# Kernel optimization log

Hardware: AMD Instinct MI355X
Metric: run time of the kernel (lower is better)

Reference implementation:

```python
import jax, jax.numpy as jnp
import numpy as np

B, T, C, H, N = 2, 1024, 1024, 16, 64
D_DECAY, D_AAA, D_MV, D_GATE = 64, 64, 32, 128
LN_EPS = 64e-5  # GroupNorm eps used by RWKV7 (1e-5 * head_size_divisor**2)


def setup_inputs():
    key = jax.random.key(0)
    ks = jax.random.split(key, 32)
    rn = lambda k, shape, s=1.0: jax.random.normal(k, shape, jnp.float32) * s
    p = {}
    p['x'] = rn(ks[0], (B, T, C))
    p['v_first'] = rn(ks[1], (B, T, C))
    for i, nm in enumerate(['x_r', 'x_w', 'x_k', 'x_v', 'x_a', 'x_g']):
        p[nm] = jax.random.uniform(ks[2 + i], (1, 1, C), jnp.float32)
    p['w1'] = rn(ks[8], (C, D_DECAY), 0.02); p['w2'] = rn(ks[9], (D_DECAY, C), 0.02); p['w0'] = rn(ks[10], (C,), 0.5)
    p['a1'] = rn(ks[11], (C, D_AAA), 0.02); p['a2'] = rn(ks[12], (D_AAA, C), 0.02); p['a0'] = rn(ks[13], (C,), 0.1)
    p['v1'] = rn(ks[14], (C, D_MV), 0.02); p['v2'] = rn(ks[15], (D_MV, C), 0.02); p['v0'] = rn(ks[16], (C,), 0.1)
    p['g1'] = rn(ks[17], (C, D_GATE), 0.02); p['g2'] = rn(ks[18], (D_GATE, C), 0.02)
    p['k_k'] = jax.random.uniform(ks[19], (1, 1, C), jnp.float32)
    p['k_a'] = jax.random.uniform(ks[20], (1, 1, C), jnp.float32)
    p['r_k'] = rn(ks[21], (H, N), 0.1)
    s = C ** -0.5
    p['W_r'] = rn(ks[22], (C, C), s); p['W_k'] = rn(ks[23], (C, C), s)
    p['W_v'] = rn(ks[24], (C, C), s); p['W_o'] = rn(ks[25], (C, C), s)
    p['ln_w'] = jnp.ones((C,), jnp.float32); p['ln_b'] = jnp.zeros((C,), jnp.float32)
    return p


def _rwkv7_op(r, w, k, v, a, b):
    # r,w,k,v,a,b: (B,T,C). Per-head matrix-state recurrence:
    #   S_t = S_{t-1} * diag(decay_t) + (S_{t-1} @ a_t) b_t^T + v_t k_t^T ; out_t = S_t @ r_t
    f = lambda z: z.reshape(B, T, H, N).astype(jnp.float32).transpose(1, 0, 2, 3)  # (T,B,H,N)
    r_, k_, v_, a_, b_ = f(r), f(k), f(v), f(a), f(b)
    d_ = jnp.exp(-jnp.exp(f(w)))  # decay in (0,1)

    def step(S, inp):
        rt, dt, kt, vt, at, bt = inp  # each (B,H,N)
        sa = jnp.einsum('bhij,bhj->bhi', S, at)
        S = S * dt[:, :, None, :] + sa[..., None] * bt[:, :, None, :] + vt[..., None] * kt[:, :, None, :]
        return S, jnp.einsum('bhij,bhj->bhi', S, rt)

    S0 = jnp.zeros((B, H, N, N), jnp.float32)
    _, out = jax.lax.scan(step, S0, (r_, d_, k_, v_, a_, b_))
    return out.transpose(1, 0, 2, 3).reshape(B, T, C)


def _forward(x, v_first, x_r, x_w, x_k, x_v, x_a, x_g, w1, w2, w0, a1, a2, a0,
             v1, v2, v0, g1, g2, k_k, k_a, r_k, W_r, W_k, W_v, W_o, ln_w, ln_b):
    xx = jnp.pad(x, ((0, 0), (1, 0), (0, 0)))[:, :T] - x  # token shift
    xr = x + xx * x_r; xw = x + xx * x_w; xk = x + xx * x_k
    xv = x + xx * x_v; xa = x + xx * x_a; xg = x + xx * x_g
    r = xr @ W_r
    w = -jax.nn.softplus(-(jnp.tanh(xw @ w1) @ w2 + w0)) - 0.5
    k = xk @ W_k
    v = xv @ W_v
    v = v + (v_first - v) * jax.nn.sigmoid(xv @ v1 @ v2 + v0)  # layer_id > 0 branch
    a = jax.nn.sigmoid(xa @ a1 @ a2 + a0)
    g = jax.nn.sigmoid(xg @ g1) @ g2
    kk = (k * k_k).reshape(B, T, H, N)
    kk = (kk / jnp.maximum(jnp.linalg.norm(kk, axis=-1, keepdims=True), 1e-12)).reshape(B, T, C)
    k = k * (1.0 + (a - 1.0) * k_a)
    y = _rwkv7_op(r, w, k, v, -kk, kk * a)
    # GroupNorm(H groups over C) applied per token
    yh = y.reshape(B, T, H, N)
    mu = yh.mean(-1, keepdims=True)
    var = yh.var(-1, keepdims=True)
    y = ((yh - mu) / jnp.sqrt(var + LN_EPS)).reshape(B, T, C) * ln_w + ln_b
    rh = r.reshape(B, T, H, N); kh = k.reshape(B, T, H, N); vh = v.reshape(B, T, H, N)
    y = y + ((rh * kh * r_k).sum(-1, keepdims=True) * vh).reshape(B, T, C)
    return (y * g) @ W_o


def reference(x, v_first, x_r, x_w, x_k, x_v, x_a, x_g, w1, w2, w0, a1, a2, a0,
              v1, v2, v0, g1, g2, k_k, k_a, r_k, W_r, W_k, W_v, W_o, ln_w, ln_b):
    out = _forward(x, v_first, x_r, x_w, x_k, x_v, x_a, x_g, w1, w2, w0, a1, a2, a0,
                   v1, v2, v0, g1, g2, k_k, k_a, r_k, W_r, W_k, W_v, W_o, ln_w, ln_b)
    return (out, v_first)
```

## Files before the change

kernel.cpp:

```cpp
#include <hip/hip_runtime.h>
#include <hip/hip_bf16.h>
#include <cstdint>
#include <cstddef>

typedef __hip_bfloat16 bf16;
typedef __bf16 bf16x8 __attribute__((ext_vector_type(8)));
typedef float f32x4 __attribute__((ext_vector_type(4)));

#define BB 2
#define TT 1024
#define CC 1024
#define HH 16
#define PKS 448
#define PKB 1792
#define CH 8
#define NCH 4
#define STEPB 2048
#define CHB (CH * STEPB)
#define NC (TT / CH)

__device__ __forceinline__ bf16 f2b(float v){ return __float2bfloat16(v); }

__device__ __forceinline__ float hex_add(float x) {
    x += __int_as_float(__builtin_amdgcn_mov_dpp(__float_as_int(x), 0xB1, 0xF, 0xF, true));
    x += __int_as_float(__builtin_amdgcn_mov_dpp(__float_as_int(x), 0x4E, 0xF, 0xF, true));
    x += __int_as_float(__builtin_amdgcn_mov_dpp(__float_as_int(x), 0x141, 0xF, 0xF, true));
    x += __int_as_float(__builtin_amdgcn_mov_dpp(__float_as_int(x), 0x140, 0xF, 0xF, true));
    return x;
}

typedef __attribute__((address_space(3))) void as3_void;
typedef __attribute__((address_space(1))) const void as1_void;
__device__ __forceinline__ void gload_lds16(const void* g, void* l) {
    __builtin_amdgcn_global_load_lds((as1_void*)g, (as3_void*)l, 16, 0, 0);
}

struct TrDesc { const float* in; bf16* out; int R, S; };
struct PrepArgs {
    TrDesc d[12];
    const float* x; const float* vfirst;
    const float *mr, *mw, *mk, *mv, *ma, *mg;
    bf16 *xr, *xw, *xk, *xv, *xa, *xg;
    float* vout;
};

__global__ __launch_bounds__(256) void prep_kernel(PrepArgs args)
{
    if (blockIdx.z < 12) {
        TrDesc t = args.d[blockIdx.z];
        __shared__ float tile[32][33];
        int s0 = blockIdx.x * 32, r0 = blockIdx.y * 32;
        if (s0 >= t.S || r0 >= t.R) return;
        int tx = threadIdx.x & 31, ty = threadIdx.x >> 5;
#pragma unroll
        for (int i = 0; i < 4; i++) {
            int r = r0 + ty + i * 8, s = s0 + tx;
            if (r < t.R && s < t.S) tile[ty + i * 8][tx] = t.in[(size_t)r * t.S + s];
        }
        __syncthreads();
#pragma unroll
        for (int i = 0; i < 4; i++) {
            int s = s0 + ty + i * 8, r = r0 + tx;
            if (s < t.S && r < t.R) t.out[(size_t)s * t.R + r] = f2b(tile[tx][ty + i * 8]);
        }
        return;
    }
    int bid = blockIdx.y * 32 + blockIdx.x;
#pragma unroll
    for (int rr = 0; rr < 2; rr++) {
        int row = bid * 2 + rr;
        int t = row & (TT - 1);
        size_t base = (size_t)row * CC;
        for (int c = threadIdx.x; c < CC; c += 256) {
            float xc = args.x[base + c];
            float xp = (t > 0) ? args.x[base - CC + c] : 0.f;
            float d = xp - xc;
            args.xr[base + c] = f2b(xc + d * args.mr[c]);
            args.xw[base + c] = f2b(xc + d * args.mw[c]);
            args.xk[base + c] = f2b(xc + d * args.mk[c]);
            args.xv[base + c] = f2b(xc + d * args.mv[c]);
            args.xa[base + c] = f2b(xc + d * args.ma[c]);
            args.xg[base + c] = f2b(xc + d * args.mg[c]);
            args.vout[base + c] = args.vfirst[base + c];
        }
    }
}

template <class EmitF>
__device__ __forceinline__ void gemm_tile(const bf16* __restrict__ A, const bf16* __restrict__ BT,
                                          int K, int m0, int n0, EmitF emit)
{
    __shared__ __align__(16) bf16 Atile[2][128 * 32];
    __shared__ __align__(16) bf16 Btile[2][128 * 32];
    int tid = threadIdx.x;
    int w = tid >> 6, lane = tid & 63;
    int wr = w >> 1, wc = w & 1;
    int quad = lane >> 4, l16 = lane & 15;

    f32x4 zero = {0.f, 0.f, 0.f, 0.f};
    f32x4 acc[4][4];
#pragma unroll
    for (int i = 0; i < 4; i++)
#pragma unroll
        for (int j = 0; j < 4; j++) acc[i][j] = zero;

    int rr = lane >> 2;
    int cs = lane & 3;
    int ra0 = w * 32 + rr;
    int ra1 = ra0 + 16;
    int cg0 = cs ^ ((ra0 >> 1) & 3);
    int cg1 = cs ^ ((ra1 >> 1) & 3);

    const bf16* Ar0 = A  + (size_t)(m0 + ra0) * K + cg0 * 8;
    const bf16* Ar1 = A  + (size_t)(m0 + ra1) * K + cg1 * 8;
    const bf16* Br0 = BT + (size_t)(n0 + ra0) * K + cg0 * 8;
    const bf16* Br1 = BT + (size_t)(n0 + ra1) * K + cg1 * 8;

    auto stage = [&](int k0, int buf) {
        bf16* atb = Atile[buf] + w * 1024;
        bf16* btb = Btile[buf] + w * 1024;
        gload_lds16(Ar0 + k0, atb);
        gload_lds16(Ar1 + k0, atb + 512);
        gload_lds16(Br0 + k0, btb);
        gload_lds16(Br1 + k0, btb + 512);
    };

    stage(0, 0);
    __syncthreads();

    int cur = 0;
    for (int k0 = 0; k0 < K; k0 += 32) {
        if (k0 + 32 < K) stage(k0 + 32, cur ^ 1);

        bf16x8 af[4], bfr[4];
#pragma unroll
        for (int mi = 0; mi < 4; mi++) {
            int m = wr * 64 + mi * 16 + l16;
            int c2 = quad ^ ((m >> 1) & 3);
            af[mi] = *reinterpret_cast<const bf16x8*>(&Atile[cur][m * 32 + c2 * 8]);
        }
#pragma unroll
        for (int ni = 0; ni < 4; ni++) {
            int n = wc * 64 + ni * 16 + l16;
            int c2 = quad ^ ((n >> 1) & 3);
            bfr[ni] = *reinterpret_cast<const bf16x8*>(&Btile[cur][n * 32 + c2 * 8]);
        }
#pragma unroll
        for (int mi = 0; mi < 4; mi++)
#pragma unroll
            for (int ni = 0; ni < 4; ni++)
                acc[mi][ni] = __builtin_amdgcn_mfma_f32_16x16x32_bf16(af[mi], bfr[ni], acc[mi][ni], 0, 0, 0);

        __syncthreads();
        cur ^= 1;
    }

#pragma unroll
    for (int mi = 0; mi < 4; mi++)
#pragma unroll
        for (int ni = 0; ni < 4; ni++)
#pragma unroll
            for (int rg = 0; rg < 4; rg++) {
                int m = m0 + wr * 64 + mi * 16 + quad * 4 + rg;
                int n = n0 + wc * 64 + ni * 16 + l16;
                emit(m, n, acc[mi][ni][rg]);
            }
}

struct L1Desc { const bf16* A; const bf16* BT; bf16* outB; int N; int mode; };
struct ProjArgs { const bf16* A[3]; const bf16* BT[3]; float* out[3]; L1Desc d[4]; };

__global__ __launch_bounds__(256) void proj_kernel(ProjArgs args)
{
    int z = blockIdx.z;
    if (z < 3) {
        float* out = args.out[z];
        gemm_tile(args.A[z], args.BT[z], 1024, blockIdx.x * 128, blockIdx.y * 128,
                  [&](int m, int n, float v) { out[(size_t)m * 1024 + n] = v; });
        return;
    }
    if (blockIdx.y) return;
    L1Desc dz = args.d[z - 3];
    gemm_tile(dz.A, dz.BT, 1024, blockIdx.x * 128, 0,
              [&](int m, int n, float v) {
                  if (n < dz.N) {
                      float r = (dz.mode == 2) ? tanhf(v)
                              : (dz.mode == 3) ? 1.f / (1.f + expf(-v)) : v;
                      dz.outB[(size_t)m * dz.N + n] = f2b(r);
                  }
              });
}

struct L2Desc { const bf16* A; const bf16* BT; const float* bias; float* outF; int K; int mode; };
struct L2Args { L2Desc d[4]; const float* vraw; const float* vfirst; };
__global__ __launch_bounds__(256) void lora2_kernel(L2Args args)
{
    L2Desc dz = args.d[blockIdx.z];
    gemm_tile(dz.A, dz.BT, dz.K, blockIdx.x * 128, blockIdx.y * 128,
              [&](int m, int n, float v) {
                  size_t idx = (size_t)m * 1024 + n;
                  if (dz.mode == 4) {
                      float xx = v + dz.bias[n];
                      float ww = -log1pf(expf(-xx)) - 0.5f;
                      dz.outF[idx] = expf(-expf(ww));
                  } else if (dz.mode == 5) {
                      float xx = v + dz.bias[n];
                      dz.outF[idx] = 1.f / (1.f + expf(-xx));
                  } else if (dz.mode == 6) {
                      float gate = 1.f / (1.f + expf(-(v + dz.bias[n])));
                      float vr = args.vraw[idx];
                      dz.outF[idx] = vr + (args.vfirst[idx] - vr) * gate;
                  } else {
                      dz.outF[idx] = v;
                  }
              });
}

__global__ __launch_bounds__(256) void final_kernel(const bf16* __restrict__ A, const bf16* __restrict__ BT,
                                                    float* __restrict__ out)
{
    gemm_tile(A, BT, 1024, blockIdx.x * 128, blockIdx.y * 128,
              [&](int m, int n, float v) { out[(size_t)m * 1024 + n] = v; });
}

__global__ __launch_bounds__(256) void pack_kernel(
    float* __restrict__ k, const float* __restrict__ a, const float* __restrict__ r,
    const float* __restrict__ v, const float* __restrict__ dw,
    const float* __restrict__ kkw, const float* __restrict__ kaw,
    float* __restrict__ PK)
{
    int tid = threadIdx.x;
    int wave = tid >> 6, lane = tid & 63;
    int idx = blockIdx.x * 4 + wave;
    size_t off = (size_t)idx * 64 + lane;
    int c = (idx & 15) * 64 + lane;
    float kraw = k[off];
    float av = a[off];
    float kkv = kraw * kkw[c];
    float s = kkv * kkv;
#pragma unroll
    for (int m = 32; m; m >>= 1) s += __shfl_xor(s, m);
    float kkn = kkv / fmaxf(sqrtf(s), 1e-12f);
    float ks = kraw * (1.f + (av - 1.f) * kaw[c]);
    k[off] = ks;
    float bb = kkn * av;
    float rv = r[off];
    float dv = dw[off];
    float bt = bb * rv, ct = ks * rv;
#pragma unroll
    for (int m = 32; m; m >>= 1) { bt += __shfl_xor(bt, m); ct += __shfl_xor(ct, m); }
    int b = idx >> 14;
    int h = idx & 15;
    int t = (idx >> 4) & (TT - 1);
    size_t sidx = (size_t)(b * HH + h) * TT + t;
    float* pw = PK + sidx * PKS;
    pw[lane] = ks; pw[64 + lane] = kkn; pw[128 + lane] = bb; pw[192 + lane] = v[off];
    pw[256 + lane] = rv; pw[320 + lane] = dv;
    if (lane == 0) { pw[384] = bt; pw[385] = ct; }
}

struct SetR { f32x4 q, d, r, k, b; float vi; float2 bc; };

__device__ __forceinline__ void ds_load_set(SetR& s, const char* slot, int c16, int row)
{
    s.q  = *(const f32x4*)(slot + 256  + c16);
    s.d  = *(const f32x4*)(slot + 1280 + c16);
    s.r  = *(const f32x4*)(slot + 1024 + c16);
    s.k  = *(const f32x4*)(slot + 0    + c16);
    s.b  = *(const f32x4*)(slot + 512  + c16);
    s.vi = *(const float*)(slot + 768 + row * 4);
    s.bc = *(const float2*)(slot + 1536);
}

__device__ __forceinline__ float step4(const SetR& sd, f32x4& S)
{
    f32x4 Sd   = S * sd.d;
    f32x4 sacv = S * sd.q;
    f32x4 oacv = Sd * sd.r;
    float sar = (sacv[0] + sacv[1]) + (sacv[2] + sacv[3]);
    float od  = (oacv[0] + oacv[1]) + (oacv[2] + oacv[3]);
    sar = hex_add(sar);
    od  = hex_add(od);
    float sa = -sar;
    float o = fmaf(sd.vi, sd.bc.y, fmaf(sa, sd.bc.x, od));
    S = Sd + sa * sd.b + sd.vi * sd.k;
    return o;
}

__global__ __launch_bounds__(256, 1) void scan_kernel(
    const float* __restrict__ PK, float* __restrict__ ybuf)
{
    __shared__ __align__(16) char ring[NCH * CHB];
    const int tid = threadIdx.x;
    const int wid = tid >> 6, lane = tid & 63;
    const int xcd = blockIdx.x & 7, kk = blockIdx.x >> 3;
    const int bh = xcd * 4 + (kk >> 4);
    const int wq = kk & 15;
    const int b = bh >> 4, h = bh & 15;
    const int row = wq * 4 + (lane >> 4);
    const int c = lane & 15;
    const int c16 = c * 16;

    const char* base = (const char*)(PK + (size_t)bh * TT * PKS);
    const char* g1 = base + lane * 16;
    const char* g2 = g1 + 1024;

    auto stage_chunk = [&](int ci) {
        const char* p1 = g1 + (size_t)ci * CH * PKB;
        const char* p2 = g2 + (size_t)ci * CH * PKB;
        char* s = ring + (ci & (NCH - 1)) * CHB;
        for (int j = wid - 1; j < CH; j += 3) {
            gload_lds16(p1 + (size_t)j * PKB, s + j * STEPB);
            gload_lds16(p2 + (size_t)j * PKB, s + j * STEPB + 1024);
        }
    };

    if (wid > 0) {
        stage_chunk(0);
        stage_chunk(1);
        stage_chunk(2);
        asm volatile("s_waitcnt vmcnt(0)" ::: "memory");
    }
    __builtin_amdgcn_sched_barrier(0);
    __builtin_amdgcn_s_barrier();
    __builtin_amdgcn_sched_barrier(0);

    f32x4 S = {0.f, 0.f, 0.f, 0.f};
    SetR X, Y;
    if (wid == 0) ds_load_set(X, ring, c16, row);
    float* py = ybuf + (size_t)b * TT * CC + h * 64 + row;

    for (int i = 0; i < NC; i++) {
        if (wid == 0) {
            const char* sl  = ring + (i & (NCH - 1)) * CHB;
            const char* sln = ring + ((i + 1) & (NCH - 1)) * CHB;
            float o;
            ds_load_set(Y, sl + 1 * STEPB, c16, row); o = step4(X, S); if (c == 0) *py = o; py += CC;
            ds_load_set(X, sl + 2 * STEPB, c16, row); o = step4(Y, S); if (c == 0) *py = o; py += CC;
            ds_load_set(Y, sl + 3 * STEPB, c16, row); o = step4(X, S); if (c == 0) *py = o; py += CC;
            ds_load_set(X, sl + 4 * STEPB, c16, row); o = step4(Y, S); if (c == 0) *py = o; py += CC;
            ds_load_set(Y, sl + 5 * STEPB, c16, row); o = step4(X, S); if (c == 0) *py = o; py += CC;
            ds_load_set(X, sl + 6 * STEPB, c16, row); o = step4(Y, S); if (c == 0) *py = o; py += CC;
            ds_load_set(Y, sl + 7 * STEPB, c16, row); o = step4(X, S); if (c == 0) *py = o; py += CC;
            ds_load_set(X, sln,            c16, row); o = step4(Y, S); if (c == 0) *py = o; py += CC;
        } else {
            if (i + 3 < NC) {
                stage_chunk(i + 3);
                if (wid == 3) asm volatile("s_waitcnt vmcnt(4)" ::: "memory");
                else          asm volatile("s_waitcnt vmcnt(6)" ::: "memory");
            } else {
                asm volatile("s_waitcnt vmcnt(0)" ::: "memory");
            }
        }
        __builtin_amdgcn_sched_barrier(0);
        __builtin_amdgcn_s_barrier();
        __builtin_amdgcn_sched_barrier(0);
    }
}

__global__ __launch_bounds__(256) void gn_kernel(
    const float* __restrict__ y, const float* __restrict__ r, const float* __restrict__ k,
    const float* __restrict__ v, const float* __restrict__ g,
    const float* __restrict__ lnw, const float* __restrict__ lnb,
    const float* __restrict__ rk, bf16* __restrict__ z)
{
    int tid = threadIdx.x;
    int idx = blockIdx.x * 4 + (tid >> 6);
    int lane = tid & 63;
    size_t off = (size_t)idx * 64 + lane;
    int c = (idx & 15) * 64 + lane;
    float yv = y[off];
    float rv = r[off], kv = k[off], vv = v[off];
    float s1 = yv, s2 = yv * yv, s3 = rv * kv * rk[c];
#pragma unroll
    for (int m = 32; m; m >>= 1) {
        s1 += __shfl_xor(s1, m);
        s2 += __shfl_xor(s2, m);
        s3 += __shfl_xor(s3, m);
    }
    float mu = s1 * (1.f / 64.f);
    float var = fmaxf(s2 * (1.f / 64.f) - mu * mu, 0.f);
    float yn = (yv - mu) * rsqrtf(var + 64e-5f) * lnw[c] + lnb[c];
    float out = (yn + s3 * vv) * g[off];
    z[off] = f2b(out);
}

extern "C" void kernel_launch(void* const* d_in, const int* in_sizes, int n_in,
                              void* d_out, int out_size, void* d_ws, size_t ws_size,
                              hipStream_t stream)
{
    const float* x       = (const float*)d_in[0];
    const float* v_first = (const float*)d_in[1];
    const float* x_r = (const float*)d_in[2];
    const float* x_w = (const float*)d_in[3];
    const float* x_k = (const float*)d_in[4];
    const float* x_v = (const float*)d_in[5];
    const float* x_a = (const float*)d_in[6];
    const float* x_g = (const float*)d_in[7];
    const float* w1 = (const float*)d_in[8];
    const float* w2 = (const float*)d_in[9];
    const float* w0 = (const float*)d_in[10];
    const float* a1 = (const float*)d_in[11];
    const float* a2 = (const float*)d_in[12];
    const float* a0 = (const float*)d_in[13];
    const float* v1 = (const float*)d_in[14];
    const float* v2 = (const float*)d_in[15];
    const float* v0 = (const float*)d_in[16];
    const float* g1 = (const float*)d_in[17];
    const float* g2 = (const float*)d_in[18];
    const float* k_k = (const float*)d_in[19];
    const float* k_a = (const float*)d_in[20];
    const float* r_k = (const float*)d_in[21];
    const float* W_r = (const float*)d_in[22];
    const float* W_k = (const float*)d_in[23];
    const float* W_v = (const float*)d_in[24];
    const float* W_o = (const float*)d_in[25];
    const float* ln_w = (const float*)d_in[26];
    const float* ln_b = (const float*)d_in[27];

    const size_t BTC = (size_t)BB * TT * CC;
    const int M = BB * TT;

    char* ws = (char*)d_ws;
    size_t off = 0;
    auto alloc = [&](size_t bytes) -> char* {
        char* p = ws + off;
        off += (bytes + 255) & ~(size_t)255;
        return p;
    };

    bf16* xr = (bf16*)alloc(BTC * 2);
    bf16* xw = (bf16*)alloc(BTC * 2);
    bf16* xk = (bf16*)alloc(BTC * 2);
    bf16* xv = (bf16*)alloc(BTC * 2);
    bf16* xa = (bf16*)alloc(BTC * 2);
    bf16* xg = (bf16*)alloc(BTC * 2);
    bf16* WrT = (bf16*)alloc(1024 * 1024 * 2);
    bf16* WkT = (bf16*)alloc(1024 * 1024 * 2);
    bf16* WvT = (bf16*)alloc(1024 * 1024 * 2);
    bf16* w1T = (bf16*)alloc(128 * 1024 * 2);
    bf16* a1T = (bf16*)alloc(128 * 1024 * 2);
    bf16* v1T = (bf16*)alloc(128 * 1024 * 2);
    bf16* g1T = (bf16*)alloc(128 * 1024 * 2);
    bf16* w2T = (bf16*)alloc(1024 * 64 * 2);
    bf16* a2T = (bf16*)alloc(1024 * 64 * 2);
    bf16* v2T = (bf16*)alloc(1024 * 32 * 2);
    bf16* g2T = (bf16*)alloc(1024 * 128 * 2);
    bf16* h_w = (bf16*)alloc((size_t)M * 64 * 2);
    bf16* h_a = (bf16*)alloc((size_t)M * 64 * 2);
    bf16* h_v = (bf16*)alloc((size_t)M * 32 * 2);
    bf16* h_g = (bf16*)alloc((size_t)M * 128 * 2);

    float* PK = (float*)ws;
    size_t pk_end = (size_t)BB * HH * TT * PKS * 4;
    if (off < pk_end) off = pk_end;
    off = (off + 255) & ~(size_t)255;

    bf16* WoT = (bf16*)alloc(1024 * 1024 * 2);
    float* rbuf = (float*)alloc(BTC * 4);
    float* kbuf = (float*)alloc(BTC * 4);
    float* vraw = (float*)alloc(BTC * 4);
    float* vbuf = (float*)alloc(BTC * 4);
    float* dbuf = (float*)alloc(BTC * 4);
    float* abuf = (float*)alloc(BTC * 4);
    float* gbuf = (float*)alloc(BTC * 4);

    float* ybuf = vraw;
    bf16*  zbuf = (bf16*)dbuf;

    (void)in_sizes; (void)n_in; (void)out_size; (void)ws_size;

    PrepArgs pa;
    pa.d[0]  = {W_r, WrT, 1024, 1024};
    pa.d[1]  = {W_k, WkT, 1024, 1024};
    pa.d[2]  = {W_v, WvT, 1024, 1024};
    pa.d[3]  = {W_o, WoT, 1024, 1024};
    pa.d[4]  = {w1, w1T, 1024, 64};
    pa.d[5]  = {a1, a1T, 1024, 64};
    pa.d[6]  = {v1, v1T, 1024, 32};
    pa.d[7]  = {g1, g1T, 1024, 128};
    pa.d[8]  = {w2, w2T, 64, 1024};
    pa.d[9]  = {a2, a2T, 64, 1024};
    pa.d[10] = {v2, v2T, 32, 1024};
    pa.d[11] = {g2, g2T, 128, 1024};
    pa.x = x; pa.vfirst = v_first;
    pa.mr = x_r; pa.mw = x_w; pa.mk = x_k; pa.mv = x_v; pa.ma = x_a; pa.mg = x_g;
    pa.xr = xr; pa.xw = xw; pa.xk = xk; pa.xv = xv; pa.xa = xa; pa.xg = xg;
    pa.vout = (float*)d_out + BTC;
    prep_kernel<<<dim3(32, 32, 13), 256, 0, stream>>>(pa);

    ProjArgs pj;
    pj.A[0] = xr; pj.A[1] = xk; pj.A[2] = xv;
    pj.BT[0] = WrT; pj.BT[1] = WkT; pj.BT[2] = WvT;
    pj.out[0] = rbuf; pj.out[1] = kbuf; pj.out[2] = vraw;
    pj.d[0] = {xw, w1T, h_w, 64, 2};
    pj.d[1] = {xa, a1T, h_a, 64, 0};
    pj.d[2] = {xv, v1T, h_v, 32, 0};
    pj.d[3] = {xg, g1T, h_g, 128, 3};
    proj_kernel<<<dim3(16, 8, 7), 256, 0, stream>>>(pj);

    L2Args l2;
    l2.d[0] = {h_w, w2T, w0, dbuf, 64, 4};
    l2.d[1] = {h_a, a2T, a0, abuf, 64, 5};
    l2.d[2] = {h_v, v2T, v0, vbuf, 32, 6};
    l2.d[3] = {h_g, g2T, nullptr, gbuf, 128, 0};
    l2.vraw = vraw; l2.vfirst = v_first;
    lora2_kernel<<<dim3(16, 8, 4), 256, 0, stream>>>(l2);

    pack_kernel<<<BB * TT * HH / 4, 256, 0, stream>>>(kbuf, abuf, rbuf, vbuf, dbuf, k_k, k_a, PK);

    scan_kernel<<<BB * HH * 16, 256, 0, stream>>>(PK, ybuf);

    gn_kernel<<<BB * TT * HH / 4, 256, 0, stream>>>(ybuf, rbuf, kbuf, vbuf, gbuf, ln_w, ln_b, r_k, zbuf);

    final_kernel<<<dim3(16, 8), 256, 0, stream>>>(zbuf, WoT, (float*)d_out);
}
```

Baseline: 412.8 us.

## Split scan state across two compute waves with two loader waves

The recurrence scan now uses two compute wavefronts instead of one. Each lane holds 2 state columns instead of 4, and 32 lanes cover a row, with an extra shfl_xor step to finish each reduction. The global-to-LDS staging moves from three producer waves to two, and the vmcnt waits are adjusted to match. This shortens the per-step serial arithmetic chain in the latency-bound scan, at the cost of an extra cross-lane shuffle per reduction and fewer loader waves.

```diff
diff --git a/kernel.cpp b/kernel.cpp
--- a/kernel.cpp
+++ b/kernel.cpp
@@ -6,6 +6,7 @@
 typedef __hip_bfloat16 bf16;
 typedef __bf16 bf16x8 __attribute__((ext_vector_type(8)));
 typedef float f32x4 __attribute__((ext_vector_type(4)));
+typedef float f32x2 __attribute__((ext_vector_type(2)));
 
 #define BB 2
 #define TT 1024
@@ -259,28 +260,28 @@
     if (lane == 0) { pw[384] = bt; pw[385] = ct; }
 }
 
-struct SetR { f32x4 q, d, r, k, b; float vi; float2 bc; };
-
-__device__ __forceinline__ void ds_load_set(SetR& s, const char* slot, int c16, int row)
-{
-    s.q  = *(const f32x4*)(slot + 256  + c16);
-    s.d  = *(const f32x4*)(slot + 1280 + c16);
-    s.r  = *(const f32x4*)(slot + 1024 + c16);
-    s.k  = *(const f32x4*)(slot + 0    + c16);
-    s.b  = *(const f32x4*)(slot + 512  + c16);
+struct SetR2 { f32x2 q, d, r, k, b; float vi; float2 bc; };
+
+__device__ __forceinline__ void ds_load_set2(SetR2& s, const char* slot, int c8, int row)
+{
+    s.q  = *(const f32x2*)(slot + 256  + c8);
+    s.d  = *(const f32x2*)(slot + 1280 + c8);
+    s.r  = *(const f32x2*)(slot + 1024 + c8);
+    s.k  = *(const f32x2*)(slot + 0    + c8);
+    s.b  = *(const f32x2*)(slot + 512  + c8);
     s.vi = *(const float*)(slot + 768 + row * 4);
     s.bc = *(const float2*)(slot + 1536);
 }
 
-__device__ __forceinline__ float step4(const SetR& sd, f32x4& S)
-{
-    f32x4 Sd   = S * sd.d;
-    f32x4 sacv = S * sd.q;
-    f32x4 oacv = Sd * sd.r;
-    float sar = (sacv[0] + sacv[1]) + (sacv[2] + sacv[3]);
-    float od  = (oacv[0] + oacv[1]) + (oacv[2] + oacv[3]);
-    sar = hex_add(sar);
-    od  = hex_add(od);
+__device__ __forceinline__ float step2(const SetR2& sd, f32x2& S)
+{
+    f32x2 Sd   = S * sd.d;
+    f32x2 sacv = S * sd.q;
+    f32x2 oacv = Sd * sd.r;
+    float sar = sacv[0] + sacv[1];
+    float od  = oacv[0] + oacv[1];
+    sar = hex_add(sar); sar += __shfl_xor(sar, 16);
+    od  = hex_add(od);  od  += __shfl_xor(od, 16);
     float sa = -sar;
     float o = fmaf(sd.vi, sd.bc.y, fmaf(sa, sd.bc.x, od));
     S = Sd + sa * sd.b + sd.vi * sd.k;
@@ -297,9 +298,9 @@
     const int bh = xcd * 4 + (kk >> 4);
     const int wq = kk & 15;
     const int b = bh >> 4, h = bh & 15;
-    const int row = wq * 4 + (lane >> 4);
-    const int c = lane & 15;
-    const int c16 = c * 16;
+    const int row = wq * 4 + wid * 2 + (lane >> 5);
+    const int c = lane & 31;
+    const int c8 = c * 8;
 
     const char* base = (const char*)(PK + (size_t)bh * TT * PKS);
     const char* g1 = base + lane * 16;
@@ -309,13 +310,13 @@
         const char* p1 = g1 + (size_t)ci * CH * PKB;
         const char* p2 = g2 + (size_t)ci * CH * PKB;
         char* s = ring + (ci & (NCH - 1)) * CHB;
-        for (int j = wid - 1; j < CH; j += 3) {
+        for (int j = wid - 2; j < CH; j += 2) {
             gload_lds16(p1 + (size_t)j * PKB, s + j * STEPB);
             gload_lds16(p2 + (size_t)j * PKB, s + j * STEPB + 1024);
         }
     };
 
-    if (wid > 0) {
+    if (wid >= 2) {
         stage_chunk(0);
         stage_chunk(1);
         stage_chunk(2);
@@ -325,29 +326,28 @@
     __builtin_amdgcn_s_barrier();
     __builtin_amdgcn_sched_barrier(0);
 
-    f32x4 S = {0.f, 0.f, 0.f, 0.f};
-    SetR X, Y;
-    if (wid == 0) ds_load_set(X, ring, c16, row);
+    f32x2 S = {0.f, 0.f};
+    SetR2 X, Y;
+    if (wid < 2) ds_load_set2(X, ring, c8, row);
     float* py = ybuf + (size_t)b * TT * CC + h * 64 + row;
 
     for (int i = 0; i < NC; i++) {
-        if (wid == 0) {
+        if (wid < 2) {
             const char* sl  = ring + (i & (NCH - 1)) * CHB;
             const char* sln = ring + ((i + 1) & (NCH - 1)) * CHB;
             float o;
-            ds_load_set(Y, sl + 1 * STEPB, c16, row); o = step4(X, S); if (c == 0) *py = o; py += CC;
-            ds_load_set(X, sl + 2 * STEPB, c16, row); o = step4(Y, S); if (c == 0) *py = o; py += CC;
-            ds_load_set(Y, sl + 3 * STEPB, c16, row); o = step4(X, S); if (c == 0) *py = o; py += CC;
-            ds_load_set(X, sl + 4 * STEPB, c16, row); o = step4(Y, S); if (c == 0) *py = o; py += CC;
-            ds_load_set(Y, sl + 5 * STEPB, c16, row); o = step4(X, S); if (c == 0) *py = o; py += CC;
-            ds_load_set(X, sl + 6 * STEPB, c16, row); o = step4(Y, S); if (c == 0) *py = o; py += CC;
-            ds_load_set(Y, sl + 7 * STEPB, c16, row); o = step4(X, S); if (c == 0) *py = o; py += CC;
-            ds_load_set(X, sln,            c16, row); o = step4(Y, S); if (c == 0) *py = o; py += CC;
+            ds_load_set2(Y, sl + 1 * STEPB, c8, row); o = step2(X, S); if (c == 0) *py = o; py += CC;
+            ds_load_set2(X, sl + 2 * STEPB, c8, row); o = step2(Y, S); if (c == 0) *py = o; py += CC;
+            ds_load_set2(Y, sl + 3 * STEPB, c8, row); o = step2(X, S); if (c == 0) *py = o; py += CC;
+            ds_load_set2(X, sl + 4 * STEPB, c8, row); o = step2(Y, S); if (c == 0) *py = o; py += CC;
+            ds_load_set2(Y, sl + 5 * STEPB, c8, row); o = step2(X, S); if (c == 0) *py = o; py += CC;
+            ds_load_set2(X, sl + 6 * STEPB, c8, row); o = step2(Y, S); if (c == 0) *py = o; py += CC;
+            ds_load_set2(Y, sl + 7 * STEPB, c8, row); o = step2(X, S); if (c == 0) *py = o; py += CC;
+            ds_load_set2(X, sln,            c8, row); o = step2(Y, S); if (c == 0) *py = o; py += CC;
         } else {
             if (i + 3 < NC) {
                 stage_chunk(i + 3);
-                if (wid == 3) asm volatile("s_waitcnt vmcnt(4)" ::: "memory");
-                else          asm volatile("s_waitcnt vmcnt(6)" ::: "memory");
+                asm volatile("s_waitcnt vmcnt(8)" ::: "memory");
             } else {
                 asm volatile("s_waitcnt vmcnt(0)" ::: "memory");
             }
```

Result: slower. 435.6 us (+5.5%).

## Fuse two recurrence steps per scan iteration via precomputed pair coefficients

Applied to the files above, without the earlier changes.

The pack kernel now precomputes algebraically combined coefficients for pairs of consecutive timesteps (combined decay, cross terms between the two a/b vectors, merged k and r terms). The scan kernel then advances the state two tokens per iteration, with three reductions plus one for the second output instead of two reductions per token. This halves the number of serial state updates on the latency-bound single-wave scan path. In exchange, each staged record is larger (768 floats per pair), the pack kernel does more shuffles and arithmetic, and rounding differs from the step-by-step update.

```diff
diff --git a/kernel.cpp b/kernel.cpp
--- a/kernel.cpp
+++ b/kernel.cpp
@@ -11,13 +11,12 @@
 #define TT 1024
 #define CC 1024
 #define HH 16
-#define PKS 448
-#define PKB 1792
-#define CH 8
+#define NP 512
+#define PRB 3072
+#define CH 4
 #define NCH 4
-#define STEPB 2048
-#define CHB (CH * STEPB)
-#define NC (TT / CH)
+#define CHB (CH * PRB)
+#define NC (NP / CH)
 
 __device__ __forceinline__ bf16 f2b(float v){ return __float2bfloat16(v); }
 
@@ -232,59 +231,83 @@
     int tid = threadIdx.x;
     int wave = tid >> 6, lane = tid & 63;
     int idx = blockIdx.x * 4 + wave;
-    size_t off = (size_t)idx * 64 + lane;
-    int c = (idx & 15) * 64 + lane;
-    float kraw = k[off];
-    float av = a[off];
-    float kkv = kraw * kkw[c];
-    float s = kkv * kkv;
-#pragma unroll
-    for (int m = 32; m; m >>= 1) s += __shfl_xor(s, m);
-    float kkn = kkv / fmaxf(sqrtf(s), 1e-12f);
-    float ks = kraw * (1.f + (av - 1.f) * kaw[c]);
-    k[off] = ks;
-    float bb = kkn * av;
-    float rv = r[off];
-    float dv = dw[off];
-    float bt = bb * rv, ct = ks * rv;
-#pragma unroll
-    for (int m = 32; m; m >>= 1) { bt += __shfl_xor(bt, m); ct += __shfl_xor(ct, m); }
-    int b = idx >> 14;
-    int h = idx & 15;
-    int t = (idx >> 4) & (TT - 1);
-    size_t sidx = (size_t)(b * HH + h) * TT + t;
-    float* pw = PK + sidx * PKS;
-    pw[lane] = ks; pw[64 + lane] = kkn; pw[128 + lane] = bb; pw[192 + lane] = v[off];
-    pw[256 + lane] = rv; pw[320 + lane] = dv;
-    if (lane == 0) { pw[384] = bt; pw[385] = ct; }
-}
-
-struct SetR { f32x4 q, d, r, k, b; float vi; float2 bc; };
-
-__device__ __forceinline__ void ds_load_set(SetR& s, const char* slot, int c16, int row)
-{
-    s.q  = *(const f32x4*)(slot + 256  + c16);
-    s.d  = *(const f32x4*)(slot + 1280 + c16);
-    s.r  = *(const f32x4*)(slot + 1024 + c16);
-    s.k  = *(const f32x4*)(slot + 0    + c16);
-    s.b  = *(const f32x4*)(slot + 512  + c16);
-    s.vi = *(const float*)(slot + 768 + row * 4);
-    s.bc = *(const float2*)(slot + 1536);
-}
-
-__device__ __forceinline__ float step4(const SetR& sd, f32x4& S)
-{
-    f32x4 Sd   = S * sd.d;
-    f32x4 sacv = S * sd.q;
-    f32x4 oacv = Sd * sd.r;
-    float sar = (sacv[0] + sacv[1]) + (sacv[2] + sacv[3]);
-    float od  = (oacv[0] + oacv[1]) + (oacv[2] + oacv[3]);
-    sar = hex_add(sar);
-    od  = hex_add(od);
-    float sa = -sar;
-    float o = fmaf(sd.vi, sd.bc.y, fmaf(sa, sd.bc.x, od));
-    S = Sd + sa * sd.b + sd.vi * sd.k;
-    return o;
+    int b  = idx >> 13;
+    int tp = (idx >> 4) & (NP - 1);
+    int h  = idx & 15;
+    size_t off0 = ((size_t)(b * TT + 2 * tp) * HH + h) * 64 + lane;
+    size_t off1 = off0 + 1024;
+    float kkw_l = kkw[h * 64 + lane];
+    float kaw_l = kaw[h * 64 + lane];
+
+    float k0 = k[off0], a0 = a[off0], r0 = r[off0], v0 = v[off0], d0 = dw[off0];
+    float k1 = k[off1], a1 = a[off1], r1 = r[off1], v1 = v[off1], d1 = dw[off1];
+
+    float kk0 = k0 * kkw_l, kk1 = k1 * kkw_l;
+    float ks0 = k0 * fmaf(a0 - 1.f, kaw_l, 1.f);
+    float ks1 = k1 * fmaf(a1 - 1.f, kaw_l, 1.f);
+    k[off0] = ks0; k[off1] = ks1;
+
+    float s0 = kk0 * kk0, s1 = kk1 * kk1;
+#pragma unroll
+    for (int m = 32; m; m >>= 1) { s0 += __shfl_xor(s0, m); s1 += __shfl_xor(s1, m); }
+    float kn0 = kk0 / fmaxf(sqrtf(s0), 1e-12f);
+    float kn1 = kk1 / fmaxf(sqrtf(s1), 1e-12f);
+    float A0 = -kn0, A1 = -kn1;
+    float B0 = kn0 * a0, B1 = kn1 * a1;
+
+    float cBA = B0 * A1, cKA = ks0 * A1, beta = B0 * r0, gamma = ks0 * r0;
+#pragma unroll
+    for (int m = 32; m; m >>= 1) {
+        cBA += __shfl_xor(cBA, m); cKA += __shfl_xor(cKA, m);
+        beta += __shfl_xor(beta, m); gamma += __shfl_xor(gamma, m);
+    }
+
+    float At = fmaf(cBA, A0, d0 * A1);
+    float Bt = d1 * B0;
+    float kt = fmaf(cKA, B1, d1 * ks0);
+    float rt = d0 * r0;
+    float d2 = d0 * d1;
+
+    size_t sidx = ((size_t)(b * HH + h) * NP + tp);
+    float* pw = PK + sidx * 768;
+    pw[lane] = kt;        pw[64 + lane]  = ks1;
+    pw[128 + lane] = A0;  pw[192 + lane] = At;
+    pw[256 + lane] = Bt;  pw[320 + lane] = B1;
+    pw[384 + lane] = rt;  pw[448 + lane] = r1;
+    pw[512 + lane] = d2;  pw[576 + lane] = v0;  pw[640 + lane] = v1;
+    if (lane == 0) { pw[704] = beta; pw[705] = gamma; }
+}
+
+struct SetP { f32x4 kt, k1, A, At, Bt, B1, rt, r1, d2; float v0, v1; float2 bg; };
+
+__device__ __forceinline__ void ds_load_pair(SetP& s, const char* slot, int c16, int row)
+{
+    s.A  = *(const f32x4*)(slot + 512  + c16);
+    s.At = *(const f32x4*)(slot + 768  + c16);
+    s.rt = *(const f32x4*)(slot + 1536 + c16);
+    s.d2 = *(const f32x4*)(slot + 2048 + c16);
+    s.Bt = *(const f32x4*)(slot + 1024 + c16);
+    s.B1 = *(const f32x4*)(slot + 1280 + c16);
+    s.kt = *(const f32x4*)(slot + 0    + c16);
+    s.k1 = *(const f32x4*)(slot + 256  + c16);
+    s.r1 = *(const f32x4*)(slot + 1792 + c16);
+    s.v0 = *(const float*)(slot + 2304 + row * 4);
+    s.v1 = *(const float*)(slot + 2560 + row * 4);
+    s.bg = *(const float2*)(slot + 2816);
+}
+
+__device__ __forceinline__ void step_pair(const SetP& sd, f32x4& S, float& o1, float& o2)
+{
+    f32x4 pv = S * sd.A;
+    f32x4 qv = S * sd.At;
+    f32x4 rv = S * sd.rt;
+    float p  = hex_add((pv[0] + pv[1]) + (pv[2] + pv[3]));
+    float q  = hex_add((qv[0] + qv[1]) + (qv[2] + qv[3]));
+    float ro = hex_add((rv[0] + rv[1]) + (rv[2] + rv[3]));
+    o1 = fmaf(sd.v0, sd.bg.y, fmaf(p, sd.bg.x, ro));
+    S = S * sd.d2 + p * sd.Bt + q * sd.B1 + sd.v0 * sd.kt + sd.v1 * sd.k1;
+    f32x4 ov = S * sd.r1;
+    o2 = hex_add((ov[0] + ov[1]) + (ov[2] + ov[3]));
 }
 
 __global__ __launch_bounds__(256, 1) void scan_kernel(
@@ -301,17 +324,16 @@
     const int c = lane & 15;
     const int c16 = c * 16;
 
-    const char* base = (const char*)(PK + (size_t)bh * TT * PKS);
-    const char* g1 = base + lane * 16;
-    const char* g2 = g1 + 1024;
+    const char* base = (const char*)(PK + (size_t)bh * NP * 768);
+    const char* gl = base + lane * 16;
 
     auto stage_chunk = [&](int ci) {
-        const char* p1 = g1 + (size_t)ci * CH * PKB;
-        const char* p2 = g2 + (size_t)ci * CH * PKB;
-        char* s = ring + (ci & (NCH - 1)) * CHB;
         for (int j = wid - 1; j < CH; j += 3) {
-            gload_lds16(p1 + (size_t)j * PKB, s + j * STEPB);
-            gload_lds16(p2 + (size_t)j * PKB, s + j * STEPB + 1024);
+            const char* p = gl + (size_t)(ci * CH + j) * PRB;
+            char* s = ring + (ci & (NCH - 1)) * CHB + j * PRB;
+            gload_lds16(p,        s);
+            gload_lds16(p + 1024, s + 1024);
+            gload_lds16(p + 2048, s + 2048);
         }
     };
 
@@ -326,28 +348,32 @@
     __builtin_amdgcn_sched_barrier(0);
 
     f32x4 S = {0.f, 0.f, 0.f, 0.f};
-    SetR X, Y;
-    if (wid == 0) ds_load_set(X, ring, c16, row);
+    SetP X, Y;
+    if (wid == 0) ds_load_pair(X, ring, c16, row);
     float* py = ybuf + (size_t)b * TT * CC + h * 64 + row;
 
     for (int i = 0; i < NC; i++) {
         if (wid == 0) {
             const char* sl  = ring + (i & (NCH - 1)) * CHB;
             const char* sln = ring + ((i + 1) & (NCH - 1)) * CHB;
-            float o;
-            ds_load_set(Y, sl + 1 * STEPB, c16, row); o = step4(X, S); if (c == 0) *py = o; py += CC;
-            ds_load_set(X, sl + 2 * STEPB, c16, row); o = step4(Y, S); if (c == 0) *py = o; py += CC;
-            ds_load_set(Y, sl + 3 * STEPB, c16, row); o = step4(X, S); if (c == 0) *py = o; py += CC;
-            ds_load_set(X, sl + 4 * STEPB, c16, row); o = step4(Y, S); if (c == 0) *py = o; py += CC;
-            ds_load_set(Y, sl + 5 * STEPB, c16, row); o = step4(X, S); if (c == 0) *py = o; py += CC;
-            ds_load_set(X, sl + 6 * STEPB, c16, row); o = step4(Y, S); if (c == 0) *py = o; py += CC;
-            ds_load_set(Y, sl + 7 * STEPB, c16, row); o = step4(X, S); if (c == 0) *py = o; py += CC;
-            ds_load_set(X, sln,            c16, row); o = step4(Y, S); if (c == 0) *py = o; py += CC;
+            float o1, o2;
+            ds_load_pair(Y, sl + 1 * PRB, c16, row);
+            step_pair(X, S, o1, o2);
+            if (c == 0) { py[0] = o1; py[CC] = o2; } py += 2 * CC;
+            ds_load_pair(X, sl + 2 * PRB, c16, row);
+            step_pair(Y, S, o1, o2);
+            if (c == 0) { py[0] = o1; py[CC] = o2; } py += 2 * CC;
+            ds_load_pair(Y, sl + 3 * PRB, c16, row);
+            step_pair(X, S, o1, o2);
+            if (c == 0) { py[0] = o1; py[CC] = o2; } py += 2 * CC;
+            ds_load_pair(X, sln, c16, row);
+            step_pair(Y, S, o1, o2);
+            if (c == 0) { py[0] = o1; py[CC] = o2; } py += 2 * CC;
         } else {
             if (i + 3 < NC) {
                 stage_chunk(i + 3);
-                if (wid == 3) asm volatile("s_waitcnt vmcnt(4)" ::: "memory");
-                else          asm volatile("s_waitcnt vmcnt(6)" ::: "memory");
+                if (wid == 1) asm volatile("s_waitcnt vmcnt(6)" ::: "memory");
+                else          asm volatile("s_waitcnt vmcnt(3)" ::: "memory");
             } else {
                 asm volatile("s_waitcnt vmcnt(0)" ::: "memory");
             }
@@ -452,7 +478,7 @@
     bf16* h_g = (bf16*)alloc((size_t)M * 128 * 2);
 
     float* PK = (float*)ws;
-    size_t pk_end = (size_t)BB * HH * TT * PKS * 4;
+    size_t pk_end = (size_t)BB * HH * NP * PRB;
     if (off < pk_end) off = pk_end;
     off = (off + 255) & ~(size_t)255;
 
@@ -507,7 +533,7 @@
     l2.vraw = vraw; l2.vfirst = v_first;
     lora2_kernel<<<dim3(16, 8, 4), 256, 0, stream>>>(l2);
 
-    pack_kernel<<<BB * TT * HH / 4, 256, 0, stream>>>(kbuf, abuf, rbuf, vbuf, dbuf, k_k, k_a, PK);
+    pack_kernel<<<BB * NP * HH / 4, 256, 0, stream>>>(kbuf, abuf, rbuf, vbuf, dbuf, k_k, k_a, PK);
 
     scan_kernel<<<BB * HH * 16, 256, 0, stream>>>(PK, ybuf);
 
```

New measurement: 535.3 us. 1.3x slower.
